# Optimization experiments

Measured on AMD Instinct MI355X. Metric: run time of the kernel, lower is better.

The kernel has to match this reference:

```python
import jax, jax.numpy as jnp
import numpy as np

N = 300000
N_LEVELS = 16
FPL = 2            # n_features_per_level
BASE = 16          # base_resolution
LOG2_T = 19       # log2_hashmap_size
T = 1 << LOG2_T
NEURONS = 64
ENC_DIM = N_LEVELS * FPL  # 32
PRIMES = np.array([1, 2654435761, 805459861, 3674653429], dtype=np.uint32)


def hash_encode(x4, table):
    """Multi-resolution 4D hash-grid encoding (tcnn HashGrid, per_level_scale=2).
    x4: [N,4] in [0,1]; table: [L, T, FPL]. Returns [N, L*FPL]."""
    xc = jnp.clip(x4, 0.0, 1.0)
    feats = []
    for l in range(N_LEVELS):
        scale = BASE * (2.0 ** l) - 1.0
        pos = xc * scale + 0.5
        p0 = jnp.floor(pos)
        w = pos - p0                      # [N,4] interp weights
        p0i = p0.astype(jnp.uint32)
        acc = jnp.zeros((x4.shape[0], FPL), dtype=table.dtype)
        for c in range(16):               # 16 hypercube corners
            off = np.array([(c >> d) & 1 for d in range(4)], dtype=np.uint32)
            idx = p0i + off               # [N,4] uint32
            h = ((idx[:, 0] * PRIMES[0]) ^ (idx[:, 1] * PRIMES[1])
                 ^ (idx[:, 2] * PRIMES[2]) ^ (idx[:, 3] * PRIMES[3]))
            h = (h & jnp.uint32(T - 1)).astype(jnp.int32)
            wsel = jnp.where(off.astype(bool), w, 1.0 - w)
            wc = wsel.prod(axis=1)        # [N]
            acc = acc + table[l][h] * wc[:, None]
        feats.append(acc)
    return jnp.concatenate(feats, axis=-1)


def mlp_head(x, W0, W1, W2):
    # FullyFusedMLP: 2 hidden ReLU layers, linear output, no biases
    h = jax.nn.relu(x @ W0)
    h = jax.nn.relu(h @ W1)
    return h @ W2


def setup_inputs() -> dict:
    ks = jax.random.split(jax.random.key(0), 32)
    d = {
        'xyz': jax.random.normal(ks[0], (N, 3), jnp.float32),
        'scales': jax.random.normal(ks[1], (N, 3), jnp.float32),
        'rotations': jax.random.normal(ks[2], (N, 4), jnp.float32),
        'opacity': jax.random.normal(ks[3], (N, 1), jnp.float32),
        'shs': jax.random.normal(ks[4], (N, 16, 3), jnp.float32),
        'time': jax.random.uniform(ks[5], (N, 1), jnp.float32),
        'xyz_bound_min': jnp.full((3,), -2.0, jnp.float32),
        'xyz_bound_max': jnp.full((3,), 2.0, jnp.float32),
        'hash_table': jax.random.uniform(ks[6], (N_LEVELS, T, FPL), jnp.float32, -1e-4, 1e-4),
        'W_enc0': jax.random.normal(ks[7], (ENC_DIM, NEURONS), jnp.float32) * 0.1,
        'W_enc1': jax.random.normal(ks[8], (NEURONS, NEURONS), jnp.float32) * 0.1,
    }
    outs = {'xyz': 3, 'scl': 3, 'rot': 4, 'op': 1, 'shs': 48}
    i = 9
    for name, od in outs.items():
        d[f'W_{name}0'] = jax.random.normal(ks[i], (NEURONS, NEURONS), jnp.float32) * 0.1
        d[f'W_{name}1'] = jax.random.normal(ks[i + 1], (NEURONS, NEURONS), jnp.float32) * 0.1
        d[f'W_{name}2'] = jax.random.normal(ks[i + 2], (NEURONS, od), jnp.float32) * 0.1
        i += 3
    return d


def reference(xyz, scales, rotations, opacity, shs, time,
              xyz_bound_min, xyz_bound_max, hash_table,
              W_enc0, W_enc1,
              W_xyz0, W_xyz1, W_xyz2,
              W_scl0, W_scl1, W_scl2,
              W_rot0, W_rot1, W_rot2,
              W_op0, W_op1, W_op2,
              W_shs0, W_shs1, W_shs2):
    # get_contracted_xyz runs under no_grad in the original
    contracted = jax.lax.stop_gradient(
        (xyz - xyz_bound_min) / (xyz_bound_max - xyz_bound_min))
    mask = jnp.all((contracted >= 0) & (contracted <= 1), axis=1)  # [N]
    x4 = jnp.concatenate([contracted, time], axis=-1)              # [N,4]
    enc = hash_encode(x4, hash_table)                              # [N,32]
    # enc_model network: 1 hidden layer, ReLU output activation
    hidden = jax.nn.relu(jax.nn.relu(enc @ W_enc0) @ W_enc1)       # [N,64]
    d_xyz = mlp_head(hidden, W_xyz0, W_xyz1, W_xyz2)
    d_rot = mlp_head(hidden, W_rot0, W_rot1, W_rot2)
    d_scl = mlp_head(hidden, W_scl0, W_scl1, W_scl2)
    d_op = mlp_head(hidden, W_op0, W_op1, W_op2)
    d_shs = mlp_head(hidden, W_shs0, W_shs1, W_shs2).reshape(-1, 16, 3)
    m1 = mask[:, None]
    new_xyz = jnp.where(m1, xyz + d_xyz, xyz)
    new_rot = jnp.where(m1, rotations + d_rot, rotations)
    new_scales = jnp.where(m1, scales + d_scl, scales)
    new_opacity = jnp.where(m1, opacity + d_op, opacity)
    new_shs = jnp.where(mask[:, None, None], shs + d_shs, shs)
    return (new_xyz, new_scales, new_rot, new_opacity, new_shs)
```

## Files before the change

### kernel.cpp

```cpp
#include <hip/hip_runtime.h>

#define NPTS 300000
#define LOG2T 19
#define TSIZE (1u<<LOG2T)
#define NROWS 300032u
#define BLKS_PER_LV 1172u

typedef float f32x4 __attribute__((ext_vector_type(4)));
typedef __bf16 bf16x8 __attribute__((ext_vector_type(8)));

__device__ __forceinline__ unsigned short f2bf(float f){
  unsigned u = __builtin_bit_cast(unsigned, f);
  u += 0x7fffu + ((u>>16)&1u);
  return (unsigned short)(u>>16);
}
__device__ __forceinline__ float bf_lo(unsigned v){ return __builtin_bit_cast(float, v<<16); }
__device__ __forceinline__ float bf_hi(unsigned v){ return __builtin_bit_cast(float, v&0xffff0000u); }

struct WP { const float* p[17]; };

__device__ const int LK[17]  = {32,64, 64,64,64, 64,64,64, 64,64,64, 64,64,64, 64,64,64};
__device__ const int LN[17]  = {64,64, 64,64, 3, 64,64, 3, 64,64, 4, 64,64, 1, 64,64,48};
__device__ const int LNT[17] = { 4, 4,  4, 4, 1,  4, 4, 1,  4, 4, 1,  4, 4, 1,  4, 4, 3};
__device__ const int LOFF[17]= {0,4096, 12288,20480,28672, 30720,38912,47104,
                                49152,57344,65536, 67584,75776,83968, 86016,94208,102400};

__global__ void prep_all(WP wp, unsigned short* wdst,
                         const float* __restrict__ t, unsigned* __restrict__ tdst){
  int gtid = blockIdx.x*blockDim.x + threadIdx.x;
  int gstr = blockDim.x*gridDim.x;
  if(tdst){
    int n = (16 << LOG2T) / 2;
    for(int i=gtid; i<n; i+=gstr){
      float4 f = ((const float4*)t)[i];
      uint2 o;
      o.x = (unsigned)f2bf(f.x) | ((unsigned)f2bf(f.y)<<16);
      o.y = (unsigned)f2bf(f.z) | ((unsigned)f2bf(f.w)<<16);
      ((uint2*)tdst)[i] = o;
    }
  }
  for(int layer=0; layer<17; layer++){
    const float* W = wp.p[layer];
    int K = LK[layer], Nn = LN[layer], NT = LNT[layer];
    unsigned short* d = wdst + LOFF[layer]/2;
    int nel = (K/32) * NT * 512;
    for(int i=gtid; i<nel; i += gstr){
      int j = i & 7, l = (i>>3)&63, fidx = i>>9;
      int kt = fidx / NT, nt = fidx - kt*NT;
      int k = kt*32 + ((l>>4)<<3) + j;
      int n = nt*16 + (l&15);
      unsigned short v = 0;
      if(n < Nn) v = f2bf(W[k*Nn + n]);
      d[i] = v;
    }
  }
}

template<bool BT>
__global__ __launch_bounds__(256) void encode_lv(
    const float* __restrict__ xyz, const float* __restrict__ timep,
    const float* __restrict__ bmin, const float* __restrict__ bmax,
    const void* __restrict__ tab, unsigned* __restrict__ enc_t)
{
  unsigned bid = blockIdx.x;
  unsigned lv = bid / BLKS_PER_LV;
  unsigned p = (bid - lv*BLKS_PER_LV)*256u + threadIdx.x;
  size_t oidx = (size_t)lv*NROWS + p;
  if(p >= NPTS){ enc_t[oidx] = 0u; return; }

  float m0=bmin[0], m1=bmin[1], m2=bmin[2];
  float M0=bmax[0], M1=bmax[1], M2=bmax[2];
  float c0 = fminf(fmaxf((xyz[3*p  ]-m0)/(M0-m0),0.f),1.f);
  float c1 = fminf(fmaxf((xyz[3*p+1]-m1)/(M1-m1),0.f),1.f);
  float c2 = fminf(fmaxf((xyz[3*p+2]-m2)/(M2-m2),0.f),1.f);
  float c3 = fminf(fmaxf(timep[p],0.f),1.f);

  float sc = (float)(16<<lv) - 1.0f;
  float pos0 = c0*sc + 0.5f, pos1 = c1*sc + 0.5f;
  float pos2 = c2*sc + 0.5f, pos3 = c3*sc + 0.5f;
  float f0 = floorf(pos0), f1 = floorf(pos1), f2 = floorf(pos2), f3 = floorf(pos3);
  float w0 = pos0-f0, w1 = pos1-f1, w2 = pos2-f2, w3 = pos3-f3;
  unsigned i0 = (unsigned)f0, i1 = (unsigned)f1, i2 = (unsigned)f2, i3 = (unsigned)f3;
  unsigned hy0 = i1*2654435761u,     hy1 = hy0 + 2654435761u;
  unsigned hz0 = i2*805459861u,      hz1 = hz0 + 805459861u;
  unsigned ht0 = i3*3674653429u,     ht1 = ht0 + 3674653429u;
  float u0=1.f-w0, u1=1.f-w1, u2=1.f-w2, u3=1.f-w3;
  float a0 = 0.f, a1 = 0.f;
  if(BT){
    const unsigned* tb = (const unsigned*)tab + ((size_t)lv<<LOG2T);
    unsigned rh[8], va[8], vb[8];
    #pragma unroll
    for(int cc=0;cc<8;cc++){
      unsigned r = ((cc&1)?hy1:hy0) ^ ((cc&2)?hz1:hz0) ^ ((cc&4)?ht1:ht0);
      rh[cc] = r;
      unsigned h0 = (i0 ^ r) & (TSIZE-1u);
      uint2 v2 = *(const uint2*)(tb + (h0 & ~1u));
      va[cc] = (h0&1u)? v2.y : v2.x;
      vb[cc] = (h0&1u)? v2.x : v2.y;
    }
    if(i0 & 1u){
      unsigned i0p = i0 + 1u;
      #pragma unroll
      for(int cc=0;cc<8;cc++)
        vb[cc] = tb[(i0p ^ rh[cc]) & (TSIZE-1u)];
    }
    float wyz[4] = {u1*u2, w1*u2, u1*w2, w1*w2};
    #pragma unroll
    for(int cc=0;cc<8;cc++){
      float wr = wyz[cc&3] * ((cc&4)? w3 : u3);
      float wa = u0*wr, wb = w0*wr;
      a0 = fmaf(bf_lo(va[cc]), wa, a0);
      a1 = fmaf(bf_hi(va[cc]), wa, a1);
      a0 = fmaf(bf_lo(vb[cc]), wb, a0);
      a1 = fmaf(bf_hi(vb[cc]), wb, a1);
    }
  } else {
    unsigned hx0 = i0, hx1 = i0 + 1u;
    float wxy[4] = {u0*u1, w0*u1, u0*w1, w0*w1};
    float wzt[4] = {u2*u3, w2*u3, u2*w3, w2*w3};
    const float* tb = (const float*)tab + ((size_t)lv<<(LOG2T+1));
    float2 v[16];
    #pragma unroll
    for(int cc=0;cc<16;cc++){
      unsigned h = ((cc&1)?hx1:hx0) ^ ((cc&2)?hy1:hy0) ^ ((cc&4)?hz1:hz0) ^ ((cc&8)?ht1:ht0);
      v[cc] = *(const float2*)(tb + ((size_t)(h&(TSIZE-1u))<<1));
    }
    #pragma unroll
    for(int cc=0;cc<16;cc++){
      float wc = wxy[cc&3]*wzt[cc>>2];
      a0 = fmaf(v[cc].x, wc, a0);
      a1 = fmaf(v[cc].y, wc, a1);
    }
  }
  enc_t[oidx] = (unsigned)f2bf(a0) | ((unsigned)f2bf(a1)<<16);
}

__device__ __forceinline__ void pack_redist(const f32x4* acc, int addr_lo, int addr_hi,
                                            bool qhi, bf16x8* out){
  unsigned P[4][2];
  #pragma unroll
  for(int mt=0;mt<4;mt++){
    #pragma unroll
    for(int s=0;s<2;s++){
      float x = fmaxf(acc[mt][2*s  ], 0.f);
      float y = fmaxf(acc[mt][2*s+1], 0.f);
      unsigned pk;
      asm("v_cvt_pk_bf16_f32 %0, %1, %2" : "=v"(pk) : "v"(x), "v"(y));
      P[mt][s] = pk;
    }
  }
  #pragma unroll
  for(int kt=0;kt<2;kt++){
    unsigned w[4];
    #pragma unroll
    for(int t=0;t<4;t++){
      int addr = (t<2) ? addr_lo : addr_hi;
      unsigned lo = (unsigned)__builtin_amdgcn_ds_bpermute(addr, (int)P[2*kt  ][t&1]);
      unsigned hi = (unsigned)__builtin_amdgcn_ds_bpermute(addr, (int)P[2*kt+1][t&1]);
      w[t] = qhi ? hi : lo;
    }
    out[kt] = __builtin_bit_cast(bf16x8, uint4{w[0],w[1],w[2],w[3]});
  }
}

template<int MT>
__device__ __forceinline__ void head_tail(const bf16x8* bh, const char* hb,
    const float* __restrict__ resid, float* __restrict__ outp, int od,
    int p, int q, int lane, int addr_lo, int addr_hi, bool qhi, float m){
  f32x4 acc[4];
  const bf16x8* w0 = (const bf16x8*)hb;
  #pragma unroll
  for(int mt=0;mt<4;mt++){
    f32x4 a = f32x4{0.f,0.f,0.f,0.f};
    #pragma unroll
    for(int kt=0;kt<2;kt++)
      a = __builtin_amdgcn_mfma_f32_16x16x32_bf16(w0[(kt*4+mt)*64+lane], bh[kt], a, 0,0,0);
    acc[mt] = a;
  }
  bf16x8 bx[2];
  pack_redist(acc, addr_lo, addr_hi, qhi, bx);

  const bf16x8* w1 = (const bf16x8*)(hb + 8192);
  #pragma unroll
  for(int mt=0;mt<4;mt++){
    f32x4 a = f32x4{0.f,0.f,0.f,0.f};
    #pragma unroll
    for(int kt=0;kt<2;kt++)
      a = __builtin_amdgcn_mfma_f32_16x16x32_bf16(w1[(kt*4+mt)*64+lane], bx[kt], a, 0,0,0);
    acc[mt] = a;
  }
  bf16x8 by[2];
  pack_redist(acc, addr_lo, addr_hi, qhi, by);

  const bf16x8* w2 = (const bf16x8*)(hb + 16384);
  f32x4 af[MT];
  #pragma unroll
  for(int mt=0;mt<MT;mt++){
    f32x4 a = f32x4{0.f,0.f,0.f,0.f};
    #pragma unroll
    for(int kt=0;kt<2;kt++)
      a = __builtin_amdgcn_mfma_f32_16x16x32_bf16(w2[(kt*MT+mt)*64+lane], by[kt], a, 0,0,0);
    af[mt] = a;
  }
  if(p < NPTS){
    #pragma unroll
    for(int mt=0;mt<MT;mt++){
      #pragma unroll
      for(int rr=0;rr<4;rr++){
        int n = 16*mt + 4*q + rr;
        if(n < od){
          size_t idx = (size_t)p*od + n;
          outp[idx] = resid[idx] + m*af[mt][rr];
        }
      }
    }
  }
}

__global__ __launch_bounds__(256,3) void mlp_k(
    const float* __restrict__ xyz, const float* __restrict__ scales,
    const float* __restrict__ rots, const float* __restrict__ opac,
    const float* __restrict__ shs,
    const float* __restrict__ bmin, const float* __restrict__ bmax,
    const unsigned* __restrict__ enc_t, const unsigned short* __restrict__ wsw,
    float* __restrict__ out)
{
  __shared__ __align__(16) char smem[49152];
  const int tid  = threadIdx.x;
  const int lane = tid & 63;
  const int wid  = blockIdx.x*4 + (tid>>6);
  const int pb   = wid*16;
  const int q = lane>>4, r = lane&15;
  const int p = pb + r;
  const int addr_lo = (32*(q&1) + r)*4;
  const int addr_hi = addr_lo + 64;
  const bool qhi = (q >= 2);

  float m = 0.f;
  if(p < NPTS){
    float m0=bmin[0], m1=bmin[1], m2=bmin[2];
    float M0=bmax[0], M1=bmax[1], M2=bmax[2];
    float c0 = (xyz[3*p  ]-m0)/(M0-m0);
    float c1 = (xyz[3*p+1]-m1)/(M1-m1);
    float c2 = (xyz[3*p+2]-m2)/(M2-m2);
    m = (c0>=0.f && c0<=1.f && c1>=0.f && c1<=1.f && c2>=0.f && c2<=1.f) ? 1.f : 0.f;
  }

  const char* wsb = (const char*)wsw;
  uint4* s4 = (uint4*)smem;

  {
    const uint4* src = (const uint4*)(wsb + 0);
    #pragma unroll
    for(int i=0;i<12;i++) s4[tid + 256*i] = src[tid + 256*i];
  }
  __syncthreads();

  uint4 e;
  e.x = enc_t[(size_t)(4*q+0)*NROWS + p];
  e.y = enc_t[(size_t)(4*q+1)*NROWS + p];
  e.z = enc_t[(size_t)(4*q+2)*NROWS + p];
  e.w = enc_t[(size_t)(4*q+3)*NROWS + p];
  bf16x8 b0 = __builtin_bit_cast(bf16x8, e);

  f32x4 acc[4];
  const bf16x8* wf0 = (const bf16x8*)(smem + 0);
  #pragma unroll
  for(int mt=0;mt<4;mt++)
    acc[mt] = __builtin_amdgcn_mfma_f32_16x16x32_bf16(wf0[mt*64+lane], b0,
                                                      f32x4{0.f,0.f,0.f,0.f}, 0,0,0);
  bf16x8 bt[2];
  pack_redist(acc, addr_lo, addr_hi, qhi, bt);

  const bf16x8* wf1 = (const bf16x8*)(smem + 4096);
  #pragma unroll
  for(int mt=0;mt<4;mt++){
    f32x4 a = f32x4{0.f,0.f,0.f,0.f};
    #pragma unroll
    for(int kt=0;kt<2;kt++)
      a = __builtin_amdgcn_mfma_f32_16x16x32_bf16(wf1[(kt*4+mt)*64+lane], bt[kt], a, 0,0,0);
    acc[mt] = a;
  }
  bf16x8 bh[2];
  pack_redist(acc, addr_lo, addr_hi, qhi, bh);

  head_tail<1>(bh, smem+12288, xyz,    out,                 3, p,q,lane, addr_lo,addr_hi,qhi, m);
  head_tail<1>(bh, smem+30720, scales, out+(size_t)3*NPTS,  3, p,q,lane, addr_lo,addr_hi,qhi, m);
  __syncthreads();

  {
    const uint4* src = (const uint4*)(wsb + 49152);
    #pragma unroll
    for(int i=0;i<9;i++) s4[tid + 256*i] = src[tid + 256*i];
  }
  __syncthreads();
  head_tail<1>(bh, smem+0,     rots,   out+(size_t)6*NPTS,  4, p,q,lane, addr_lo,addr_hi,qhi, m);
  head_tail<1>(bh, smem+18432, opac,   out+(size_t)10*NPTS, 1, p,q,lane, addr_lo,addr_hi,qhi, m);
  __syncthreads();

  {
    const uint4* src = (const uint4*)(wsb + 86016);
    #pragma unroll
    for(int i=0;i<5;i++){
      int idx = tid + 256*i;
      if(idx < 1408) s4[idx] = src[idx];
    }
  }
  __syncthreads();
  head_tail<3>(bh, smem+0,     shs,    out+(size_t)11*NPTS, 48, p,q,lane, addr_lo,addr_hi,qhi, m);
}

extern "C" void kernel_launch(void* const* d_in, const int* in_sizes, int n_in,
                              void* d_out, int out_size, void* d_ws, size_t ws_size,
                              hipStream_t stream){
  (void)in_sizes; (void)n_in; (void)out_size;
  WP wp;
  for(int i=0;i<17;i++) wp.p[i] = (const float*)d_in[9+i];
  char* ws = (char*)d_ws;
  unsigned short* wsw = (unsigned short*)ws;

  const size_t TAB_OFF   = 131072;
  const size_t TAB_BYTES = (size_t)(16u<<LOG2T) * 4;
  const size_t ENC_BYTES = (size_t)16 * NROWS * 4;
  bool bf16tab = ws_size >= TAB_OFF + TAB_BYTES + ENC_BYTES;
  size_t enc_off = bf16tab ? (TAB_OFF + TAB_BYTES) : TAB_OFF;
  unsigned* encp = (unsigned*)(ws + enc_off);

  const float* table = (const float*)d_in[8];
  unsigned* tabp = bf16tab ? (unsigned*)(ws + TAB_OFF) : nullptr;

  prep_all<<<4160,256,0,stream>>>(wp, wsw, table, tabp);

  unsigned enc_blocks = 16u * BLKS_PER_LV;
  if(bf16tab){
    encode_lv<true><<<enc_blocks,256,0,stream>>>(
        (const float*)d_in[0], (const float*)d_in[5],
        (const float*)d_in[6], (const float*)d_in[7], tabp, encp);
  } else {
    encode_lv<false><<<enc_blocks,256,0,stream>>>(
        (const float*)d_in[0], (const float*)d_in[5],
        (const float*)d_in[6], (const float*)d_in[7], table, encp);
  }

  mlp_k<<<NROWS/64, 256, 0, stream>>>(
      (const float*)d_in[0], (const float*)d_in[1], (const float*)d_in[2],
      (const float*)d_in[3], (const float*)d_in[4],
      (const float*)d_in[6], (const float*)d_in[7],
      encp, wsw, (float*)d_out);
}
```

Baseline: 344.2 us.

## Permute weight K-rows to eliminate ds_bpermute redistribution between MLP layers

Instead of shuffling MFMA output fragments across lanes with ds_bpermute so they match the next layer's B-operand layout, the weight preparation permutes the K index of every non-first layer via a tau mapping. Each lane can then pack its own accumulator values directly into the next layer's input fragment. This removes 16 bpermute ops per layer transition across the whole MLP chain. It relies on the permutation exactly matching the MFMA 16x16x32 register layout, which must hold for correctness.

```diff
diff --git a/kernel.cpp b/kernel.cpp
--- a/kernel.cpp
+++ b/kernel.cpp
@@ -16,6 +16,10 @@
 }
 __device__ __forceinline__ float bf_lo(unsigned v){ return __builtin_bit_cast(float, v<<16); }
 __device__ __forceinline__ float bf_hi(unsigned v){ return __builtin_bit_cast(float, v&0xffff0000u); }
+
+__device__ __forceinline__ int tau(int k){
+  return 16*(2*(k>>5) + (k&1)) + 4*((k>>3)&3) + ((k>>1)&3);
+}
 
 struct WP { const float* p[17]; };
 
@@ -48,6 +52,7 @@
       int j = i & 7, l = (i>>3)&63, fidx = i>>9;
       int kt = fidx / NT, nt = fidx - kt*NT;
       int k = kt*32 + ((l>>4)<<3) + j;
+      if(layer != 0) k = tau(k);
       int n = nt*16 + (l&15);
       unsigned short v = 0;
       if(n < Nn) v = f2bf(W[k*Nn + n]);
@@ -135,29 +140,15 @@
   enc_t[oidx] = (unsigned)f2bf(a0) | ((unsigned)f2bf(a1)<<16);
 }
 
-__device__ __forceinline__ void pack_redist(const f32x4* acc, int addr_lo, int addr_hi,
-                                            bool qhi, bf16x8* out){
-  unsigned P[4][2];
-  #pragma unroll
-  for(int mt=0;mt<4;mt++){
-    #pragma unroll
-    for(int s=0;s<2;s++){
-      float x = fmaxf(acc[mt][2*s  ], 0.f);
-      float y = fmaxf(acc[mt][2*s+1], 0.f);
-      unsigned pk;
-      asm("v_cvt_pk_bf16_f32 %0, %1, %2" : "=v"(pk) : "v"(x), "v"(y));
-      P[mt][s] = pk;
-    }
-  }
+__device__ __forceinline__ void pack_local(const f32x4* acc, bf16x8* out){
   #pragma unroll
   for(int kt=0;kt<2;kt++){
     unsigned w[4];
     #pragma unroll
     for(int t=0;t<4;t++){
-      int addr = (t<2) ? addr_lo : addr_hi;
-      unsigned lo = (unsigned)__builtin_amdgcn_ds_bpermute(addr, (int)P[2*kt  ][t&1]);
-      unsigned hi = (unsigned)__builtin_amdgcn_ds_bpermute(addr, (int)P[2*kt+1][t&1]);
-      w[t] = qhi ? hi : lo;
+      float x = fmaxf(acc[2*kt  ][t], 0.f);
+      float y = fmaxf(acc[2*kt+1][t], 0.f);
+      asm("v_cvt_pk_bf16_f32 %0, %1, %2" : "=v"(w[t]) : "v"(x), "v"(y));
     }
     out[kt] = __builtin_bit_cast(bf16x8, uint4{w[0],w[1],w[2],w[3]});
   }
@@ -166,7 +157,7 @@
 template<int MT>
 __device__ __forceinline__ void head_tail(const bf16x8* bh, const char* hb,
     const float* __restrict__ resid, float* __restrict__ outp, int od,
-    int p, int q, int lane, int addr_lo, int addr_hi, bool qhi, float m){
+    int p, int q, int lane, float m){
   f32x4 acc[4];
   const bf16x8* w0 = (const bf16x8*)hb;
   #pragma unroll
@@ -178,7 +169,7 @@
     acc[mt] = a;
   }
   bf16x8 bx[2];
-  pack_redist(acc, addr_lo, addr_hi, qhi, bx);
+  pack_local(acc, bx);
 
   const bf16x8* w1 = (const bf16x8*)(hb + 8192);
   #pragma unroll
@@ -190,7 +181,7 @@
     acc[mt] = a;
   }
   bf16x8 by[2];
-  pack_redist(acc, addr_lo, addr_hi, qhi, by);
+  pack_local(acc, by);
 
   const bf16x8* w2 = (const bf16x8*)(hb + 16384);
   f32x4 af[MT];
@@ -232,9 +223,6 @@
   const int pb   = wid*16;
   const int q = lane>>4, r = lane&15;
   const int p = pb + r;
-  const int addr_lo = (32*(q&1) + r)*4;
-  const int addr_hi = addr_lo + 64;
-  const bool qhi = (q >= 2);
 
   float m = 0.f;
   if(p < NPTS){
@@ -270,7 +258,7 @@
     acc[mt] = __builtin_amdgcn_mfma_f32_16x16x32_bf16(wf0[mt*64+lane], b0,
                                                       f32x4{0.f,0.f,0.f,0.f}, 0,0,0);
   bf16x8 bt[2];
-  pack_redist(acc, addr_lo, addr_hi, qhi, bt);
+  pack_local(acc, bt);
 
   const bf16x8* wf1 = (const bf16x8*)(smem + 4096);
   #pragma unroll
@@ -282,10 +270,10 @@
     acc[mt] = a;
   }
   bf16x8 bh[2];
-  pack_redist(acc, addr_lo, addr_hi, qhi, bh);
-
-  head_tail<1>(bh, smem+12288, xyz,    out,                 3, p,q,lane, addr_lo,addr_hi,qhi, m);
-  head_tail<1>(bh, smem+30720, scales, out+(size_t)3*NPTS,  3, p,q,lane, addr_lo,addr_hi,qhi, m);
+  pack_local(acc, bh);
+
+  head_tail<1>(bh, smem+12288, xyz,    out,                 3, p,q,lane, m);
+  head_tail<1>(bh, smem+30720, scales, out+(size_t)3*NPTS,  3, p,q,lane, m);
   __syncthreads();
 
   {
@@ -294,8 +282,8 @@
     for(int i=0;i<9;i++) s4[tid + 256*i] = src[tid + 256*i];
   }
   __syncthreads();
-  head_tail<1>(bh, smem+0,     rots,   out+(size_t)6*NPTS,  4, p,q,lane, addr_lo,addr_hi,qhi, m);
-  head_tail<1>(bh, smem+18432, opac,   out+(size_t)10*NPTS, 1, p,q,lane, addr_lo,addr_hi,qhi, m);
+  head_tail<1>(bh, smem+0,     rots,   out+(size_t)6*NPTS,  4, p,q,lane, m);
+  head_tail<1>(bh, smem+18432, opac,   out+(size_t)10*NPTS, 1, p,q,lane, m);
   __syncthreads();
 
   {
@@ -307,7 +295,7 @@
     }
   }
   __syncthreads();
-  head_tail<3>(bh, smem+0,     shs,    out+(size_t)11*NPTS, 48, p,q,lane, addr_lo,addr_hi,qhi, m);
+  head_tail<3>(bh, smem+0,     shs,    out+(size_t)11*NPTS, 48, p,q,lane, m);
 }
 
 extern "C" void kernel_launch(void* const* d_in, const int* in_sizes, int n_in,
```

Result: faster. 319.2 us (-7.3%).
